# Kernel optimization log

Measured on AMD Instinct MI355X. Metric: run time of the kernel, lower is better.

## Reference

```python
import jax, jax.numpy as jnp
import numpy as np

N_NODES = 100000
N_EDGES = 1600000
IN_CH = 128
HID = 128
N_GRAPHS = 256


def gcn_conv(x, W, b, src, dst, n_nodes):
    """PyG GCNConv: linear -> symmetric degree normalization with self-loops -> scatter-add -> bias."""
    h = x @ W  # [N, H]
    # degree (in-degree on target index) including the added self-loop
    deg = 1.0 + jax.ops.segment_sum(jnp.ones((dst.shape[0],), x.dtype), dst, num_segments=n_nodes)
    dis = deg ** -0.5  # deg >= 1, no inf guard needed
    coef = dis[src] * dis[dst]  # [E]
    agg = jax.ops.segment_sum(h[src] * coef[:, None], dst, num_segments=n_nodes)
    # self-loop contribution: h[i] * dis[i]^2 = h[i] / deg[i]
    agg = agg + h * (1.0 / deg)[:, None]
    return agg + b


def global_mean_pool(x, batch, n_graphs):
    sums = jax.ops.segment_sum(x, batch, num_segments=n_graphs)
    cnts = jax.ops.segment_sum(jnp.ones((x.shape[0],), x.dtype), batch, num_segments=n_graphs)
    return sums / jnp.maximum(cnts, 1.0)[:, None]


def setup_inputs() -> dict:
    key = jax.random.key(0)
    ks = jax.random.split(key, 8)
    x = jax.random.normal(ks[0], (N_NODES, IN_CH), dtype=jnp.float32)
    edge_index = jax.random.randint(ks[1], (2, N_EDGES), 0, N_NODES, dtype=jnp.int32)
    batch = jnp.sort(jax.random.randint(ks[2], (N_NODES,), 0, N_GRAPHS, dtype=jnp.int32))
    # glorot-ish init for weights
    s1 = (6.0 / (IN_CH + HID)) ** 0.5
    W1 = jax.random.uniform(ks[3], (IN_CH, HID), jnp.float32, -s1, s1)
    b1 = jnp.zeros((HID,), jnp.float32)
    s2 = (6.0 / (HID + HID)) ** 0.5
    W2 = jax.random.uniform(ks[4], (HID, HID), jnp.float32, -s2, s2)
    b2 = jnp.zeros((HID,), jnp.float32)
    s3 = (6.0 / (HID + 1)) ** 0.5
    Wfc = jax.random.uniform(ks[5], (HID, 1), jnp.float32, -s3, s3)
    bfc = jnp.zeros((1,), jnp.float32)
    return {"x": x, "edge_index": edge_index, "batch": batch,
            "W1": W1, "b1": b1, "W2": W2, "b2": b2, "Wfc": Wfc, "bfc": bfc}


def reference(x, edge_index, batch, W1, b1, W2, b2, Wfc, bfc):
    src, dst = edge_index[0], edge_index[1]
    h = jax.nn.relu(gcn_conv(x, W1, b1, src, dst, N_NODES))
    h = jax.nn.relu(gcn_conv(h, W2, b2, src, dst, N_NODES))
    g = global_mean_pool(h, batch, N_GRAPHS)  # [G, H]
    out = g @ Wfc + bfc  # [G, 1]
    return out.squeeze(-1)
```

## Files before the change

kernel.cpp:

```cpp
#include <hip/hip_runtime.h>
#include <hip/hip_bf16.h>

#define N_NODES 100000
#define N_EDGES 1600000
#define HID 128
#define N_GRAPHS 256

#define BSHIFT 9
#define BSIZE 512
#define NBUCK ((N_NODES + BSIZE - 1) / BSIZE)
#define BCAP 14336
#define EPB 8192
#define NBLK_A ((N_EDGES + EPB - 1) / EPB)
#define ZOFF ((uint)N_NODES << 8)

typedef unsigned int uint;
typedef unsigned short ushort;
typedef short short8 __attribute__((ext_vector_type(8)));
typedef float f32x4 __attribute__((ext_vector_type(4)));

__device__ __forceinline__ ushort f2bf_hw(float f) {
    union { __hip_bfloat16 b; ushort u; } cv;
    cv.b = __float2bfloat16(f);
    return cv.u;
}
__device__ __forceinline__ uint4 pack8(const float* r) {
    uint4 o;
    o.x = (uint)f2bf_hw(r[0]) | ((uint)f2bf_hw(r[1]) << 16);
    o.y = (uint)f2bf_hw(r[2]) | ((uint)f2bf_hw(r[3]) << 16);
    o.z = (uint)f2bf_hw(r[4]) | ((uint)f2bf_hw(r[5]) << 16);
    o.w = (uint)f2bf_hw(r[6]) | ((uint)f2bf_hw(r[7]) << 16);
    return o;
}
__device__ __forceinline__ void accp(uint4 v, float2* a) {
    a[0].x += __uint_as_float(v.x << 16);
    a[0].y += __uint_as_float(v.x & 0xFFFF0000u);
    a[1].x += __uint_as_float(v.y << 16);
    a[1].y += __uint_as_float(v.y & 0xFFFF0000u);
    a[2].x += __uint_as_float(v.z << 16);
    a[2].y += __uint_as_float(v.z & 0xFFFF0000u);
    a[3].x += __uint_as_float(v.w << 16);
    a[3].y += __uint_as_float(v.w & 0xFFFF0000u);
}

union Frag16 {
    uint4 u;
    short8 s;
    ushort h[8];
};

__global__ void init_kernel(int* __restrict__ bfill, uint4* __restrict__ Azr,
                            uint4* __restrict__ Bzr) {
    int t = threadIdx.x;
    if (t < NBUCK) bfill[t] = 0;
    if (t < 16) Azr[t] = (uint4){0, 0, 0, 0};
    else if (t < 32) Bzr[t - 16] = (uint4){0, 0, 0, 0};
}

__global__ __launch_bounds__(256) void bucket_scatter_kernel(const int* __restrict__ src,
                                                             const int* __restrict__ dst,
                                                             int* __restrict__ bfill,
                                                             uint* __restrict__ bucketed) {
    __shared__ int h[NBUCK];
    __shared__ int rb[NBUCK];
    for (int t = threadIdx.x; t < NBUCK; t += 256) h[t] = 0;
    __syncthreads();
    int base = blockIdx.x * EPB;
#pragma unroll 4
    for (int it = 0; it < EPB / 256; ++it) {
        int e = base + it * 256 + threadIdx.x;
        if (e < N_EDGES) atomicAdd(&h[dst[e] >> BSHIFT], 1);
    }
    __syncthreads();
    for (int t = threadIdx.x; t < NBUCK; t += 256) {
        rb[t] = (h[t] ? atomicAdd(&bfill[t], h[t]) : 0) + t * BCAP;
        h[t] = 0;
    }
    __syncthreads();
#pragma unroll 4
    for (int it = 0; it < EPB / 256; ++it) {
        int e = base + it * 256 + threadIdx.x;
        if (e < N_EDGES) {
            int d = dst[e];
            int b = d >> BSHIFT;
            int pos = rb[b] + atomicAdd(&h[b], 1);
            bucketed[pos] = (uint)src[e] | ((uint)(d & (BSIZE - 1)) << 17);
        }
    }
}

__global__ __launch_bounds__(256) void bucket_csr_kernel(const uint* __restrict__ bucketed,
                                                         const int* __restrict__ bfill,
                                                         int* __restrict__ degi,
                                                         int* __restrict__ rowptr,
                                                         float* __restrict__ dis,
                                                         uint* __restrict__ csrb) {
    int b = blockIdx.x;
    int beg = b * BCAP;
    int ne = bfill[b];
    __shared__ int cnt[BSIZE];
    __shared__ int fl[BSIZE];
    __shared__ int ex[BSIZE];
    __shared__ int ps[256];
    int t = threadIdx.x;
    cnt[t] = 0; cnt[t + 256] = 0;
    fl[t] = 0;  fl[t + 256] = 0;
    __syncthreads();
    for (int i = t; i < ne; i += 256) atomicAdd(&cnt[bucketed[beg + i] >> 17], 1);
    __syncthreads();
    int v0 = cnt[2 * t], v1 = cnt[2 * t + 1];
    int p0 = (v0 + 15) & ~15;
    int p1 = (v1 + 15) & ~15;
    int s = p0 + p1;
    ps[t] = s;
    __syncthreads();
    for (int off = 1; off < 256; off <<= 1) {
        int a = (t >= off) ? ps[t - off] : 0;
        __syncthreads();
        ps[t] += a;
        __syncthreads();
    }
    int e0 = ps[t] - s;
    ex[2 * t] = e0;
    ex[2 * t + 1] = e0 + p0;
    int g = b * BSIZE + 2 * t;
    if (g < N_NODES) {
        degi[g] = p0; rowptr[g] = beg + e0;
        dis[g] = rsqrtf(1.0f + (float)v0);
    }
    if (g + 1 < N_NODES) {
        degi[g + 1] = p1; rowptr[g + 1] = beg + e0 + p0;
        dis[g + 1] = rsqrtf(1.0f + (float)v1);
    }
    __syncthreads();
    for (int i = t; i < ne; i += 256) {
        uint u = bucketed[beg + i];
        int dl = u >> 17;
        int p = ex[dl] + atomicAdd(&fl[dl], 1);
        csrb[beg + p] = (u & 0x1FFFFu) << 8;
    }
    __syncthreads();
    for (int p = v0; p < p0; ++p) csrb[beg + ex[2 * t] + p] = ZOFF;
    for (int p = v1; p < p1; ++p) csrb[beg + ex[2 * t + 1] + p] = ZOFF;
}

__global__ void prep_wfrag2(const float* __restrict__ W1, const float* __restrict__ W2,
                            uint4* __restrict__ WB1, uint4* __restrict__ WB2) {
    int t = blockIdx.x * 256 + threadIdx.x;
    if (t >= 4096) return;
    const float* W = (t < 2048) ? W1 : W2;
    uint4* WB = (t < 2048) ? WB1 : WB2;
    int tt = t & 2047;
    int lane = tt & 63;
    int nt = (tt >> 6) & 7;
    int kt = tt >> 9;
    int kbase = kt * 32 + (lane >> 4) * 8;
    int col = nt * 16 + (lane & 15);
    float r[8];
#pragma unroll
    for (int j = 0; j < 8; j++) r[j] = W[(size_t)(kbase + j) * 128 + col];
    WB[tt] = pack8(r);
}

template <bool F32IN>
__global__ __launch_bounds__(256) void mgemm_kernel(const void* __restrict__ Xv,
                                                    const uint4* __restrict__ WB,
                                                    const float* __restrict__ dis,
                                                    ushort* __restrict__ Y, int M) {
    __shared__ uint4 WBs[2048];
    __shared__ ushort stage[4][16][136];
#pragma unroll
    for (int i = 0; i < 8; i++) WBs[i * 256 + threadIdx.x] = WB[i * 256 + threadIdx.x];
    __syncthreads();

    int wave = threadIdx.x >> 6;
    int lane = threadIdx.x & 63;
    int r0 = blockIdx.x * 128 + wave * 32;
    if (r0 >= M) return;

    int rowA = lane & 15;
    int ksub = (lane >> 4) * 8;

    Frag16 a[2][4];
#pragma unroll
    for (int rt = 0; rt < 2; ++rt) {
        int row = r0 + rt * 16 + rowA;
        if (F32IN) {
            const float* xr = (const float*)Xv + (size_t)row * 128;
#pragma unroll
            for (int kt = 0; kt < 4; ++kt) {
                float4 lo = *(const float4*)(xr + kt * 32 + ksub);
                float4 hi = *(const float4*)(xr + kt * 32 + ksub + 4);
                float r[8] = {lo.x, lo.y, lo.z, lo.w, hi.x, hi.y, hi.z, hi.w};
                a[rt][kt].u = pack8(r);
            }
        } else {
            const uint4* xr = (const uint4*)Xv + (size_t)row * 16;
#pragma unroll
            for (int kt = 0; kt < 4; ++kt) a[rt][kt].u = xr[kt * 4 + (lane >> 4)];
        }
    }

    f32x4 acc[2][8];
#pragma unroll
    for (int rt = 0; rt < 2; ++rt)
#pragma unroll
        for (int nt = 0; nt < 8; ++nt) acc[rt][nt] = (f32x4){0.f, 0.f, 0.f, 0.f};

#pragma unroll
    for (int kt = 0; kt < 4; ++kt) {
#pragma unroll
        for (int nt = 0; nt < 8; ++nt) {
            Frag16 b;
            b.u = WBs[(kt * 8 + nt) * 64 + lane];
            acc[0][nt] = __builtin_amdgcn_mfma_f32_16x16x32_bf16(a[0][kt].s, b.s, acc[0][nt], 0, 0, 0);
            acc[1][nt] = __builtin_amdgcn_mfma_f32_16x16x32_bf16(a[1][kt].s, b.s, acc[1][nt], 0, 0, 0);
        }
    }

    int cbase = lane & 15;
    int rbl = (lane >> 4) * 4;
    ushort* sp = &stage[wave][0][0];
    char* Yb = (char*)Y;
#pragma unroll
    for (int rt = 0; rt < 2; ++rt) {
        int r0g = r0 + rt * 16;
        int rbase = r0g + rbl;
        float d0 = dis[rbase + 0], d1 = dis[rbase + 1];
        float d2 = dis[rbase + 2], d3 = dis[rbase + 3];
#pragma unroll
        for (int nt = 0; nt < 8; ++nt) {
            int col = nt * 16 + cbase;
            sp[(rbl + 0) * 136 + col] = f2bf_hw(acc[rt][nt][0] * d0);
            sp[(rbl + 1) * 136 + col] = f2bf_hw(acc[rt][nt][1] * d1);
            sp[(rbl + 2) * 136 + col] = f2bf_hw(acc[rt][nt][2] * d2);
            sp[(rbl + 3) * 136 + col] = f2bf_hw(acc[rt][nt][3] * d3);
        }
#pragma unroll
        for (int i = 0; i < 4; ++i) {
            int idx = i * 64 + lane;
            int row = idx >> 4, c16 = idx & 15;
            uint4 v = *(const uint4*)(sp + row * 136 + c16 * 8);
            *(uint4*)(Yb + (size_t)(r0g + row) * 256 + c16 * 16) = v;
        }
    }
}

template <int POOL>
__global__ __launch_bounds__(256) void aggregate_kernel(
    const ushort* __restrict__ T, const uint* __restrict__ csrb,
    const int* __restrict__ rowptr, const int* __restrict__ degi,
    const float* __restrict__ dis, const float* __restrict__ bias,
    ushort* __restrict__ H, const float* __restrict__ Wfc,
    float* __restrict__ ndot) {
    int wave = threadIdx.x >> 6;
    int node = blockIdx.x * 4 + wave;
    int lane = threadIdx.x & 63;
    int group = lane >> 4;
    uint sub16 = (uint)(lane & 15) * 16u;

    int start = rowptr[node];
    int iters = degi[node] >> 4;
    const char* Tb = (const char*)T;

    float2 acc[4];
#pragma unroll
    for (int i = 0; i < 4; i++) acc[i] = make_float2(0.f, 0.f);

    int jb = start + group;
    for (int it = 0; it < iters; ++it, jb += 16) {
        uint o0 = csrb[jb];
        uint o1 = csrb[jb + 4];
        uint o2 = csrb[jb + 8];
        uint o3 = csrb[jb + 12];
        uint4 v0 = *(const uint4*)(Tb + (o0 + sub16));
        uint4 v1 = *(const uint4*)(Tb + (o1 + sub16));
        uint4 v2 = *(const uint4*)(Tb + (o2 + sub16));
        uint4 v3 = *(const uint4*)(Tb + (o3 + sub16));
        accp(v0, acc); accp(v1, acc); accp(v2, acc); accp(v3, acc);
    }

#pragma unroll
    for (int i = 0; i < 4; i++) {
        acc[i].x += __shfl_xor(acc[i].x, 16);
        acc[i].y += __shfl_xor(acc[i].y, 16);
        acc[i].x += __shfl_xor(acc[i].x, 32);
        acc[i].y += __shfl_xor(acc[i].y, 32);
    }

    if (group == 0) {
        uint4 sv = *(const uint4*)(Tb + (((uint)node << 8) + sub16));
        accp(sv, acc);
        float di = dis[node];
        int sub = lane & 15;
        float4 blo = ((const float4*)bias)[sub * 2];
        float4 bhi = ((const float4*)bias)[sub * 2 + 1];
        float bb[8] = {blo.x, blo.y, blo.z, blo.w, bhi.x, bhi.y, bhi.z, bhi.w};
        float r[8];
        float af[8] = {acc[0].x, acc[0].y, acc[1].x, acc[1].y,
                       acc[2].x, acc[2].y, acc[3].x, acc[3].y};
#pragma unroll
        for (int i = 0; i < 8; i++) r[i] = fmaxf(di * af[i] + bb[i], 0.f);
        if (POOL == 0) {
            ((uint4*)H)[(size_t)node * 16 + sub] = pack8(r);
        } else {
            float4 wlo = ((const float4*)Wfc)[sub * 2];
            float4 whi = ((const float4*)Wfc)[sub * 2 + 1];
            float d = r[0] * wlo.x + r[1] * wlo.y + r[2] * wlo.z + r[3] * wlo.w
                    + r[4] * whi.x + r[5] * whi.y + r[6] * whi.z + r[7] * whi.w;
            d += __shfl_xor(d, 1);
            d += __shfl_xor(d, 2);
            d += __shfl_xor(d, 4);
            d += __shfl_xor(d, 8);
            if (sub == 0) ndot[node] = d;
        }
    }
}

__global__ __launch_bounds__(64) void pool_fc_kernel(const float* __restrict__ ndot,
                                                     const int* __restrict__ batch,
                                                     const float* __restrict__ bfc,
                                                     float* __restrict__ out) {
    int g = blockIdx.x;
    int lane = threadIdx.x;
    auto lb = [&](int key) {
        int lo = 0, hi = N_NODES;
        while (lo < hi) {
            int mid = (lo + hi) >> 1;
            if (batch[mid] < key) lo = mid + 1; else hi = mid;
        }
        return lo;
    };
    int a = lb(g), b = lb(g + 1);
    float s = 0.f;
    for (int i = a + lane; i < b; i += 64) s += ndot[i];
#pragma unroll
    for (int off = 32; off > 0; off >>= 1) s += __shfl_down(s, off);
    if (lane == 0) out[g] = s / fmaxf((float)(b - a), 1.0f) + bfc[0];
}

extern "C" void kernel_launch(void* const* d_in, const int* in_sizes, int n_in,
                              void* d_out, int out_size, void* d_ws, size_t ws_size,
                              hipStream_t stream) {
    const float* x    = (const float*)d_in[0];
    const int*   eidx = (const int*)d_in[1];
    const int*   batch= (const int*)d_in[2];
    const float* W1   = (const float*)d_in[3];
    const float* b1   = (const float*)d_in[4];
    const float* W2   = (const float*)d_in[5];
    const float* b2   = (const float*)d_in[6];
    const float* Wfc  = (const float*)d_in[7];
    const float* bfc  = (const float*)d_in[8];
    float* out = (float*)d_out;

    const int* src = eidx;
    const int* dst = eidx + N_EDGES;

    size_t off = 0;
    char* base = (char*)d_ws;
    auto alloc = [&](size_t bytes) -> void* {
        void* p = base + off;
        off += (bytes + 255) & ~(size_t)255;
        return p;
    };
    int*    bfill  = (int*)alloc(NBUCK * 4);
    ushort* A      = (ushort*)alloc((size_t)(N_NODES + 1) * HID * 2);
    ushort* B      = (ushort*)alloc((size_t)(N_NODES + 1) * HID * 2);
    int*    degi   = (int*)alloc(N_NODES * 4);
    int*    rowptr = (int*)alloc(N_NODES * 4);
    float*  dis    = (float*)alloc(N_NODES * 4);
    float*  ndot   = (float*)alloc(N_NODES * 4);
    uint*   csrb   = (uint*)alloc((size_t)NBUCK * BCAP * 4);
    uint*   bucketed = (uint*)alloc((size_t)NBUCK * BCAP * 4);
    uint4*  WB1    = (uint4*)alloc(2048 * 16);
    uint4*  WB2    = (uint4*)alloc(2048 * 16);

    init_kernel<<<1, 256, 0, stream>>>(bfill,
                                       (uint4*)(A + (size_t)N_NODES * HID),
                                       (uint4*)(B + (size_t)N_NODES * HID));

    bucket_scatter_kernel<<<NBLK_A, 256, 0, stream>>>(src, dst, bfill, bucketed);
    bucket_csr_kernel<<<NBUCK, 256, 0, stream>>>(bucketed, bfill, degi, rowptr, dis, csrb);

    prep_wfrag2<<<16, 256, 0, stream>>>(W1, W2, WB1, WB2);

    int gemm_grid = (N_NODES + 127) / 128;
    int agg_grid  = N_NODES / 4;

    mgemm_kernel<true><<<gemm_grid, 256, 0, stream>>>(x, WB1, dis, A, N_NODES);
    aggregate_kernel<0><<<agg_grid, 256, 0, stream>>>(A, csrb, rowptr, degi, dis, b1, B,
                                                      Wfc, ndot);
    mgemm_kernel<false><<<gemm_grid, 256, 0, stream>>>(B, WB2, dis, A, N_NODES);
    aggregate_kernel<1><<<agg_grid, 256, 0, stream>>>(A, csrb, rowptr, degi, dis, b2, B,
                                                      Wfc, ndot);

    pool_fc_kernel<<<N_GRAPHS, 64, 0, stream>>>(ndot, batch, bfc, out);
}
```

Baseline: 227.5 us.

## Fuse aggregation with GEMM via aggregate-then-transform and degree-sorted node permutation

Reorders each GCN layer to aggregate first and apply the weight matrix afterwards, so the MFMA GEMM runs inside the aggregation kernel on 16-node tiles staged in shared memory. The separate GEMM passes and their intermediate writes and reads disappear. Nodes are sorted into degree classes through a permutation so each block handles rows with similar edge counts, and CSR row padding drops from 16 to 4 to cut wasted gathers. Initialisation and weight-fragment prep are merged into one launch, at the cost of extra small histogram, scan and permutation kernels plus a shared-memory GEMM epilogue in each aggregation block.

```diff
diff --git a/kernel.cpp b/kernel.cpp
--- a/kernel.cpp
+++ b/kernel.cpp
@@ -9,9 +9,10 @@
 #define BSHIFT 9
 #define BSIZE 512
 #define NBUCK ((N_NODES + BSIZE - 1) / BSIZE)
-#define BCAP 14336
+#define BCAP 12288
 #define EPB 8192
 #define NBLK_A ((N_EDGES + EPB - 1) / EPB)
+#define NCLS 16
 #define ZOFF ((uint)N_NODES << 8)
 
 typedef unsigned int uint;
@@ -49,105 +50,20 @@
     ushort h[8];
 };
 
-__global__ void init_kernel(int* __restrict__ bfill, uint4* __restrict__ Azr,
-                            uint4* __restrict__ Bzr) {
-    int t = threadIdx.x;
-    if (t < NBUCK) bfill[t] = 0;
-    if (t < 16) Azr[t] = (uint4){0, 0, 0, 0};
-    else if (t < 32) Bzr[t - 16] = (uint4){0, 0, 0, 0};
-}
-
-__global__ __launch_bounds__(256) void bucket_scatter_kernel(const int* __restrict__ src,
-                                                             const int* __restrict__ dst,
-                                                             int* __restrict__ bfill,
-                                                             uint* __restrict__ bucketed) {
-    __shared__ int h[NBUCK];
-    __shared__ int rb[NBUCK];
-    for (int t = threadIdx.x; t < NBUCK; t += 256) h[t] = 0;
-    __syncthreads();
-    int base = blockIdx.x * EPB;
-#pragma unroll 4
-    for (int it = 0; it < EPB / 256; ++it) {
-        int e = base + it * 256 + threadIdx.x;
-        if (e < N_EDGES) atomicAdd(&h[dst[e] >> BSHIFT], 1);
-    }
-    __syncthreads();
-    for (int t = threadIdx.x; t < NBUCK; t += 256) {
-        rb[t] = (h[t] ? atomicAdd(&bfill[t], h[t]) : 0) + t * BCAP;
-        h[t] = 0;
-    }
-    __syncthreads();
-#pragma unroll 4
-    for (int it = 0; it < EPB / 256; ++it) {
-        int e = base + it * 256 + threadIdx.x;
-        if (e < N_EDGES) {
-            int d = dst[e];
-            int b = d >> BSHIFT;
-            int pos = rb[b] + atomicAdd(&h[b], 1);
-            bucketed[pos] = (uint)src[e] | ((uint)(d & (BSIZE - 1)) << 17);
-        }
-    }
-}
-
-__global__ __launch_bounds__(256) void bucket_csr_kernel(const uint* __restrict__ bucketed,
-                                                         const int* __restrict__ bfill,
-                                                         int* __restrict__ degi,
-                                                         int* __restrict__ rowptr,
-                                                         float* __restrict__ dis,
-                                                         uint* __restrict__ csrb) {
-    int b = blockIdx.x;
-    int beg = b * BCAP;
-    int ne = bfill[b];
-    __shared__ int cnt[BSIZE];
-    __shared__ int fl[BSIZE];
-    __shared__ int ex[BSIZE];
-    __shared__ int ps[256];
-    int t = threadIdx.x;
-    cnt[t] = 0; cnt[t + 256] = 0;
-    fl[t] = 0;  fl[t + 256] = 0;
-    __syncthreads();
-    for (int i = t; i < ne; i += 256) atomicAdd(&cnt[bucketed[beg + i] >> 17], 1);
-    __syncthreads();
-    int v0 = cnt[2 * t], v1 = cnt[2 * t + 1];
-    int p0 = (v0 + 15) & ~15;
-    int p1 = (v1 + 15) & ~15;
-    int s = p0 + p1;
-    ps[t] = s;
-    __syncthreads();
-    for (int off = 1; off < 256; off <<= 1) {
-        int a = (t >= off) ? ps[t - off] : 0;
-        __syncthreads();
-        ps[t] += a;
-        __syncthreads();
-    }
-    int e0 = ps[t] - s;
-    ex[2 * t] = e0;
-    ex[2 * t + 1] = e0 + p0;
-    int g = b * BSIZE + 2 * t;
-    if (g < N_NODES) {
-        degi[g] = p0; rowptr[g] = beg + e0;
-        dis[g] = rsqrtf(1.0f + (float)v0);
-    }
-    if (g + 1 < N_NODES) {
-        degi[g + 1] = p1; rowptr[g + 1] = beg + e0 + p0;
-        dis[g + 1] = rsqrtf(1.0f + (float)v1);
-    }
-    __syncthreads();
-    for (int i = t; i < ne; i += 256) {
-        uint u = bucketed[beg + i];
-        int dl = u >> 17;
-        int p = ex[dl] + atomicAdd(&fl[dl], 1);
-        csrb[beg + p] = (u & 0x1FFFFu) << 8;
-    }
-    __syncthreads();
-    for (int p = v0; p < p0; ++p) csrb[beg + ex[2 * t] + p] = ZOFF;
-    for (int p = v1; p < p1; ++p) csrb[beg + ex[2 * t + 1] + p] = ZOFF;
-}
-
-__global__ void prep_wfrag2(const float* __restrict__ W1, const float* __restrict__ W2,
-                            uint4* __restrict__ WB1, uint4* __restrict__ WB2) {
-    int t = blockIdx.x * 256 + threadIdx.x;
-    if (t >= 4096) return;
+__global__ void setup_kernel(int* __restrict__ bfill, int* __restrict__ clshist,
+                             int* __restrict__ clsfill,
+                             uint4* __restrict__ Azr, uint4* __restrict__ Bzr,
+                             const float* __restrict__ W1, const float* __restrict__ W2,
+                             uint4* __restrict__ WB1, uint4* __restrict__ WB2) {
+    if (blockIdx.x == 0) {
+        int t = threadIdx.x;
+        if (t < NBUCK) bfill[t] = 0;
+        if (t < NCLS) { clshist[t] = 0; clsfill[t] = 0; }
+        if (t < 16) Azr[t] = (uint4){0, 0, 0, 0};
+        else if (t < 32) Bzr[t - 16] = (uint4){0, 0, 0, 0};
+        return;
+    }
+    int t = (blockIdx.x - 1) * 256 + threadIdx.x;
     const float* W = (t < 2048) ? W1 : W2;
     uint4* WB = (t < 2048) ? WB1 : WB2;
     int tt = t & 2047;
@@ -162,157 +78,249 @@
     WB[tt] = pack8(r);
 }
 
-template <bool F32IN>
-__global__ __launch_bounds__(256) void mgemm_kernel(const void* __restrict__ Xv,
-                                                    const uint4* __restrict__ WB,
+__global__ __launch_bounds__(256) void bucket_scatter_kernel(const int* __restrict__ src,
+                                                             const int* __restrict__ dst,
+                                                             int* __restrict__ bfill,
+                                                             uint* __restrict__ bucketed) {
+    __shared__ int h[NBUCK];
+    __shared__ int rb[NBUCK];
+    for (int t = threadIdx.x; t < NBUCK; t += 256) h[t] = 0;
+    __syncthreads();
+    int base = blockIdx.x * EPB;
+#pragma unroll 4
+    for (int it = 0; it < EPB / 256; ++it) {
+        int e = base + it * 256 + threadIdx.x;
+        if (e < N_EDGES) atomicAdd(&h[dst[e] >> BSHIFT], 1);
+    }
+    __syncthreads();
+    for (int t = threadIdx.x; t < NBUCK; t += 256) {
+        rb[t] = (h[t] ? atomicAdd(&bfill[t], h[t]) : 0) + t * BCAP;
+        h[t] = 0;
+    }
+    __syncthreads();
+#pragma unroll 4
+    for (int it = 0; it < EPB / 256; ++it) {
+        int e = base + it * 256 + threadIdx.x;
+        if (e < N_EDGES) {
+            int d = dst[e];
+            int b = d >> BSHIFT;
+            int pos = rb[b] + atomicAdd(&h[b], 1);
+            bucketed[pos] = (uint)src[e] | ((uint)(d & (BSIZE - 1)) << 17);
+        }
+    }
+}
+
+__global__ __launch_bounds__(256) void bucket_csr_kernel(const uint* __restrict__ bucketed,
+                                                         const int* __restrict__ bfill,
+                                                         int* __restrict__ degi,
+                                                         int* __restrict__ rowptr,
+                                                         float* __restrict__ dis,
+                                                         uint* __restrict__ csrb,
+                                                         int* __restrict__ clshist) {
+    int b = blockIdx.x;
+    int beg = b * BCAP;
+    int ne = bfill[b];
+    __shared__ int cnt[BSIZE];
+    __shared__ int fl[BSIZE];
+    __shared__ int ex[BSIZE];
+    __shared__ int ps[256];
+    __shared__ int ch[NCLS];
+    int t = threadIdx.x;
+    cnt[t] = 0; cnt[t + 256] = 0;
+    fl[t] = 0;  fl[t + 256] = 0;
+    if (t < NCLS) ch[t] = 0;
+    __syncthreads();
+    for (int i = t; i < ne; i += 256) atomicAdd(&cnt[bucketed[beg + i] >> 17], 1);
+    __syncthreads();
+    int v0 = cnt[2 * t], v1 = cnt[2 * t + 1];
+    int p0 = (v0 + 3) & ~3;
+    int p1 = (v1 + 3) & ~3;
+    int s = p0 + p1;
+    ps[t] = s;
+    __syncthreads();
+    for (int off = 1; off < 256; off <<= 1) {
+        int a = (t >= off) ? ps[t - off] : 0;
+        __syncthreads();
+        ps[t] += a;
+        __syncthreads();
+    }
+    int e0 = ps[t] - s;
+    ex[2 * t] = e0;
+    ex[2 * t + 1] = e0 + p0;
+    int g = b * BSIZE + 2 * t;
+    if (g < N_NODES) {
+        degi[g] = p0; rowptr[g] = beg + e0;
+        dis[g] = rsqrtf(1.0f + (float)v0);
+        atomicAdd(&ch[min(p0 >> 2, NCLS - 1)], 1);
+    }
+    if (g + 1 < N_NODES) {
+        degi[g + 1] = p1; rowptr[g + 1] = beg + e0 + p0;
+        dis[g + 1] = rsqrtf(1.0f + (float)v1);
+        atomicAdd(&ch[min(p1 >> 2, NCLS - 1)], 1);
+    }
+    __syncthreads();
+    if (t < NCLS && ch[t]) atomicAdd(&clshist[t], ch[t]);
+    for (int i = t; i < ne; i += 256) {
+        uint u = bucketed[beg + i];
+        int dl = u >> 17;
+        int p = ex[dl] + atomicAdd(&fl[dl], 1);
+        csrb[beg + p] = (u & 0x1FFFFu) << 8;
+    }
+    __syncthreads();
+    for (int p = v0; p < p0; ++p) csrb[beg + ex[2 * t] + p] = ZOFF;
+    for (int p = v1; p < p1; ++p) csrb[beg + ex[2 * t + 1] + p] = ZOFF;
+}
+
+__global__ void clsbase_kernel(const int* __restrict__ clshist, int* __restrict__ clsbase) {
+    if (threadIdx.x == 0) {
+        int run = 0;
+        for (int c = 0; c < NCLS; ++c) { clsbase[c] = run; run += clshist[c]; }
+    }
+}
+
+__global__ __launch_bounds__(256) void perm_kernel(const int* __restrict__ degi,
+                                                   const int* __restrict__ clsbase,
+                                                   int* __restrict__ clsfill,
+                                                   int* __restrict__ perm) {
+    __shared__ int h[NCLS];
+    __shared__ int rb[NCLS];
+    int t = threadIdx.x;
+    if (t < NCLS) h[t] = 0;
+    __syncthreads();
+    int n = blockIdx.x * 256 + t;
+    int cls = 0, myloc = 0;
+    if (n < N_NODES) {
+        cls = min(degi[n] >> 2, NCLS - 1);
+        myloc = atomicAdd(&h[cls], 1);
+    }
+    __syncthreads();
+    if (t < NCLS) rb[t] = h[t] ? (clsbase[t] + atomicAdd(&clsfill[t], h[t])) : 0;
+    __syncthreads();
+    if (n < N_NODES) perm[rb[cls] + myloc] = n;
+}
+
+__global__ __launch_bounds__(256) void xprep_kernel(const float* __restrict__ x,
                                                     const float* __restrict__ dis,
-                                                    ushort* __restrict__ Y, int M) {
-    __shared__ uint4 WBs[2048];
-    __shared__ ushort stage[4][16][136];
-#pragma unroll
-    for (int i = 0; i < 8; i++) WBs[i * 256 + threadIdx.x] = WB[i * 256 + threadIdx.x];
-    __syncthreads();
-
-    int wave = threadIdx.x >> 6;
-    int lane = threadIdx.x & 63;
-    int r0 = blockIdx.x * 128 + wave * 32;
-    if (r0 >= M) return;
-
-    int rowA = lane & 15;
-    int ksub = (lane >> 4) * 8;
-
-    Frag16 a[2][4];
-#pragma unroll
-    for (int rt = 0; rt < 2; ++rt) {
-        int row = r0 + rt * 16 + rowA;
-        if (F32IN) {
-            const float* xr = (const float*)Xv + (size_t)row * 128;
-#pragma unroll
-            for (int kt = 0; kt < 4; ++kt) {
-                float4 lo = *(const float4*)(xr + kt * 32 + ksub);
-                float4 hi = *(const float4*)(xr + kt * 32 + ksub + 4);
-                float r[8] = {lo.x, lo.y, lo.z, lo.w, hi.x, hi.y, hi.z, hi.w};
-                a[rt][kt].u = pack8(r);
-            }
-        } else {
-            const uint4* xr = (const uint4*)Xv + (size_t)row * 16;
-#pragma unroll
-            for (int kt = 0; kt < 4; ++kt) a[rt][kt].u = xr[kt * 4 + (lane >> 4)];
-        }
-    }
-
-    f32x4 acc[2][8];
-#pragma unroll
-    for (int rt = 0; rt < 2; ++rt)
-#pragma unroll
-        for (int nt = 0; nt < 8; ++nt) acc[rt][nt] = (f32x4){0.f, 0.f, 0.f, 0.f};
-
-#pragma unroll
-    for (int kt = 0; kt < 4; ++kt) {
-#pragma unroll
-        for (int nt = 0; nt < 8; ++nt) {
-            Frag16 b;
-            b.u = WBs[(kt * 8 + nt) * 64 + lane];
-            acc[0][nt] = __builtin_amdgcn_mfma_f32_16x16x32_bf16(a[0][kt].s, b.s, acc[0][nt], 0, 0, 0);
-            acc[1][nt] = __builtin_amdgcn_mfma_f32_16x16x32_bf16(a[1][kt].s, b.s, acc[1][nt], 0, 0, 0);
-        }
-    }
-
-    int cbase = lane & 15;
-    int rbl = (lane >> 4) * 4;
-    ushort* sp = &stage[wave][0][0];
-    char* Yb = (char*)Y;
-#pragma unroll
-    for (int rt = 0; rt < 2; ++rt) {
-        int r0g = r0 + rt * 16;
-        int rbase = r0g + rbl;
-        float d0 = dis[rbase + 0], d1 = dis[rbase + 1];
-        float d2 = dis[rbase + 2], d3 = dis[rbase + 3];
-#pragma unroll
-        for (int nt = 0; nt < 8; ++nt) {
-            int col = nt * 16 + cbase;
-            sp[(rbl + 0) * 136 + col] = f2bf_hw(acc[rt][nt][0] * d0);
-            sp[(rbl + 1) * 136 + col] = f2bf_hw(acc[rt][nt][1] * d1);
-            sp[(rbl + 2) * 136 + col] = f2bf_hw(acc[rt][nt][2] * d2);
-            sp[(rbl + 3) * 136 + col] = f2bf_hw(acc[rt][nt][3] * d3);
-        }
-#pragma unroll
-        for (int i = 0; i < 4; ++i) {
-            int idx = i * 64 + lane;
-            int row = idx >> 4, c16 = idx & 15;
-            uint4 v = *(const uint4*)(sp + row * 136 + c16 * 8);
-            *(uint4*)(Yb + (size_t)(r0g + row) * 256 + c16 * 16) = v;
-        }
-    }
+                                                    uint4* __restrict__ Xp) {
+    int t = blockIdx.x * 256 + threadIdx.x;
+    if (t >= N_NODES * 16) return;
+    int n = t >> 4, c16 = t & 15;
+    const float* xr = x + (size_t)n * 128 + c16 * 8;
+    float d = dis[n];
+    float4 lo = *(const float4*)xr;
+    float4 hi = *(const float4*)(xr + 4);
+    float r[8] = {d * lo.x, d * lo.y, d * lo.z, d * lo.w,
+                  d * hi.x, d * hi.y, d * hi.z, d * hi.w};
+    Xp[t] = pack8(r);
 }
 
 template <int POOL>
-__global__ __launch_bounds__(256) void aggregate_kernel(
+__global__ __launch_bounds__(256, 8) void fused_agg_kernel(
     const ushort* __restrict__ T, const uint* __restrict__ csrb,
     const int* __restrict__ rowptr, const int* __restrict__ degi,
     const float* __restrict__ dis, const float* __restrict__ bias,
+    const int* __restrict__ perm, const uint4* __restrict__ WB,
     ushort* __restrict__ H, const float* __restrict__ Wfc,
     float* __restrict__ ndot) {
+    __shared__ ushort At[16][136];
+    __shared__ float disrow[16];
+    __shared__ int nid[16];
+    __shared__ float pdot[16][4];
+
     int wave = threadIdx.x >> 6;
-    int node = blockIdx.x * 4 + wave;
     int lane = threadIdx.x & 63;
     int group = lane >> 4;
-    uint sub16 = (uint)(lane & 15) * 16u;
-
+    int sub = lane & 15;
+    uint sub16 = (uint)sub * 16u;
+    int r = wave * 4 + group;
+    int node = perm[blockIdx.x * 16 + r];
     int start = rowptr[node];
-    int iters = degi[node] >> 4;
+    int iters = degi[node] >> 2;
     const char* Tb = (const char*)T;
 
     float2 acc[4];
 #pragma unroll
     for (int i = 0; i < 4; i++) acc[i] = make_float2(0.f, 0.f);
 
-    int jb = start + group;
-    for (int it = 0; it < iters; ++it, jb += 16) {
+    int jb = start;
+    for (int it = 0; it < iters; ++it, jb += 4) {
         uint o0 = csrb[jb];
-        uint o1 = csrb[jb + 4];
-        uint o2 = csrb[jb + 8];
-        uint o3 = csrb[jb + 12];
+        uint o1 = csrb[jb + 1];
+        uint o2 = csrb[jb + 2];
+        uint o3 = csrb[jb + 3];
         uint4 v0 = *(const uint4*)(Tb + (o0 + sub16));
         uint4 v1 = *(const uint4*)(Tb + (o1 + sub16));
         uint4 v2 = *(const uint4*)(Tb + (o2 + sub16));
         uint4 v3 = *(const uint4*)(Tb + (o3 + sub16));
         accp(v0, acc); accp(v1, acc); accp(v2, acc); accp(v3, acc);
     }
-
-#pragma unroll
-    for (int i = 0; i < 4; i++) {
-        acc[i].x += __shfl_xor(acc[i].x, 16);
-        acc[i].y += __shfl_xor(acc[i].y, 16);
-        acc[i].x += __shfl_xor(acc[i].x, 32);
-        acc[i].y += __shfl_xor(acc[i].y, 32);
-    }
-
-    if (group == 0) {
+    {
         uint4 sv = *(const uint4*)(Tb + (((uint)node << 8) + sub16));
         accp(sv, acc);
         float di = dis[node];
-        int sub = lane & 15;
-        float4 blo = ((const float4*)bias)[sub * 2];
-        float4 bhi = ((const float4*)bias)[sub * 2 + 1];
-        float bb[8] = {blo.x, blo.y, blo.z, blo.w, bhi.x, bhi.y, bhi.z, bhi.w};
-        float r[8];
-        float af[8] = {acc[0].x, acc[0].y, acc[1].x, acc[1].y,
-                       acc[2].x, acc[2].y, acc[3].x, acc[3].y};
-#pragma unroll
-        for (int i = 0; i < 8; i++) r[i] = fmaxf(di * af[i] + bb[i], 0.f);
-        if (POOL == 0) {
-            ((uint4*)H)[(size_t)node * 16 + sub] = pack8(r);
-        } else {
-            float4 wlo = ((const float4*)Wfc)[sub * 2];
-            float4 whi = ((const float4*)Wfc)[sub * 2 + 1];
-            float d = r[0] * wlo.x + r[1] * wlo.y + r[2] * wlo.z + r[3] * wlo.w
-                    + r[4] * whi.x + r[5] * whi.y + r[6] * whi.z + r[7] * whi.w;
-            d += __shfl_xor(d, 1);
-            d += __shfl_xor(d, 2);
-            d += __shfl_xor(d, 4);
-            d += __shfl_xor(d, 8);
-            if (sub == 0) ndot[node] = d;
+        float rr[8] = {di * acc[0].x, di * acc[0].y, di * acc[1].x, di * acc[1].y,
+                       di * acc[2].x, di * acc[2].y, di * acc[3].x, di * acc[3].y};
+        *(uint4*)&At[r][sub * 8] = pack8(rr);
+        if (sub == 0) { disrow[r] = di; nid[r] = node; }
+    }
+    __syncthreads();
+
+    Frag16 a[4];
+    int arow = lane & 15;
+    int achunk = lane >> 4;
+#pragma unroll
+    for (int kt = 0; kt < 4; ++kt)
+        a[kt].u = *(const uint4*)&At[arow][kt * 32 + achunk * 8];
+
+    f32x4 c0 = (f32x4){0.f, 0.f, 0.f, 0.f};
+    f32x4 c1 = (f32x4){0.f, 0.f, 0.f, 0.f};
+    int nt0 = wave * 2, nt1 = wave * 2 + 1;
+#pragma unroll
+    for (int kt = 0; kt < 4; ++kt) {
+        Frag16 b0, b1;
+        b0.u = WB[(kt * 8 + nt0) * 64 + lane];
+        b1.u = WB[(kt * 8 + nt1) * 64 + lane];
+        c0 = __builtin_amdgcn_mfma_f32_16x16x32_bf16(a[kt].s, b0.s, c0, 0, 0, 0);
+        c1 = __builtin_amdgcn_mfma_f32_16x16x32_bf16(a[kt].s, b1.s, c1, 0, 0, 0);
+    }
+
+    int col0 = nt0 * 16 + sub, col1 = nt1 * 16 + sub;
+    float b0s = bias[col0], b1s = bias[col1];
+    int rq = (lane >> 4) * 4;
+
+    if (POOL == 0) {
+        __syncthreads();
+#pragma unroll
+        for (int reg = 0; reg < 4; ++reg) {
+            float sc = disrow[rq + reg];
+            At[rq + reg][col0] = f2bf_hw(fmaxf(c0[reg] + b0s, 0.f) * sc);
+            At[rq + reg][col1] = f2bf_hw(fmaxf(c1[reg] + b1s, 0.f) * sc);
+        }
+        __syncthreads();
+        int row = threadIdx.x >> 4, c16 = threadIdx.x & 15;
+        uint4 v = *(const uint4*)&At[row][c16 * 8];
+        *(uint4*)((char*)H + (((size_t)(uint)nid[row]) << 8) + c16 * 16) = v;
+    } else {
+        float wf0 = Wfc[col0], wf1 = Wfc[col1];
+        float p[4];
+#pragma unroll
+        for (int reg = 0; reg < 4; ++reg)
+            p[reg] = fmaxf(c0[reg] + b0s, 0.f) * wf0 + fmaxf(c1[reg] + b1s, 0.f) * wf1;
+#pragma unroll
+        for (int reg = 0; reg < 4; ++reg) {
+            p[reg] += __shfl_xor(p[reg], 1);
+            p[reg] += __shfl_xor(p[reg], 2);
+            p[reg] += __shfl_xor(p[reg], 4);
+            p[reg] += __shfl_xor(p[reg], 8);
+        }
+        if (sub == 0) {
+#pragma unroll
+            for (int reg = 0; reg < 4; ++reg) pdot[rq + reg][wave] = p[reg];
+        }
+        __syncthreads();
+        if (threadIdx.x < 16) {
+            int row = threadIdx.x;
+            ndot[nid[row]] = pdot[row][0] + pdot[row][1] + pdot[row][2] + pdot[row][3];
         }
     }
 }
@@ -363,36 +371,41 @@
         off += (bytes + 255) & ~(size_t)255;
         return p;
     };
-    int*    bfill  = (int*)alloc(NBUCK * 4);
-    ushort* A      = (ushort*)alloc((size_t)(N_NODES + 1) * HID * 2);
-    ushort* B      = (ushort*)alloc((size_t)(N_NODES + 1) * HID * 2);
-    int*    degi   = (int*)alloc(N_NODES * 4);
-    int*    rowptr = (int*)alloc(N_NODES * 4);
-    float*  dis    = (float*)alloc(N_NODES * 4);
-    float*  ndot   = (float*)alloc(N_NODES * 4);
-    uint*   csrb   = (uint*)alloc((size_t)NBUCK * BCAP * 4);
-    uint*   bucketed = (uint*)alloc((size_t)NBUCK * BCAP * 4);
-    uint4*  WB1    = (uint4*)alloc(2048 * 16);
-    uint4*  WB2    = (uint4*)alloc(2048 * 16);
-
-    init_kernel<<<1, 256, 0, stream>>>(bfill,
-                                       (uint4*)(A + (size_t)N_NODES * HID),
-                                       (uint4*)(B + (size_t)N_NODES * HID));
+    int*    bfill   = (int*)alloc(NBUCK * 4);
+    int*    clshist = (int*)alloc(NCLS * 4);
+    int*    clsfill = (int*)alloc(NCLS * 4);
+    int*    clsbase = (int*)alloc(NCLS * 4);
+    ushort* A       = (ushort*)alloc((size_t)(N_NODES + 1) * HID * 2);
+    ushort* B       = (ushort*)alloc((size_t)(N_NODES + 1) * HID * 2);
+    int*    degi    = (int*)alloc(N_NODES * 4);
+    int*    rowptr  = (int*)alloc(N_NODES * 4);
+    float*  dis     = (float*)alloc(N_NODES * 4);
+    float*  ndot    = (float*)alloc(N_NODES * 4);
+    int*    perm    = (int*)alloc(N_NODES * 4);
+    uint*   csrb    = (uint*)alloc((size_t)NBUCK * BCAP * 4);
+    uint*   bucketed= (uint*)alloc((size_t)NBUCK * BCAP * 4);
+    uint4*  WB1     = (uint4*)alloc(2048 * 16);
+    uint4*  WB2     = (uint4*)alloc(2048 * 16);
+
+    setup_kernel<<<17, 256, 0, stream>>>(bfill, clshist, clsfill,
+                                         (uint4*)(A + (size_t)N_NODES * HID),
+                                         (uint4*)(B + (size_t)N_NODES * HID),
+                                         W1, W2, WB1, WB2);
 
     bucket_scatter_kernel<<<NBLK_A, 256, 0, stream>>>(src, dst, bfill, bucketed);
-    bucket_csr_kernel<<<NBUCK, 256, 0, stream>>>(bucketed, bfill, degi, rowptr, dis, csrb);
-
-    prep_wfrag2<<<16, 256, 0, stream>>>(W1, W2, WB1, WB2);
-
-    int gemm_grid = (N_NODES + 127) / 128;
-    int agg_grid  = N_NODES / 4;
-
-    mgemm_kernel<true><<<gemm_grid, 256, 0, stream>>>(x, WB1, dis, A, N_NODES);
-    aggregate_kernel<0><<<agg_grid, 256, 0, stream>>>(A, csrb, rowptr, degi, dis, b1, B,
-                                                      Wfc, ndot);
-    mgemm_kernel<false><<<gemm_grid, 256, 0, stream>>>(B, WB2, dis, A, N_NODES);
-    aggregate_kernel<1><<<agg_grid, 256, 0, stream>>>(A, csrb, rowptr, degi, dis, b2, B,
-                                                      Wfc, ndot);
+    bucket_csr_kernel<<<NBUCK, 256, 0, stream>>>(bucketed, bfill, degi, rowptr, dis,
+                                                 csrb, clshist);
+    clsbase_kernel<<<1, 64, 0, stream>>>(clshist, clsbase);
+    perm_kernel<<<(N_NODES + 255) / 256, 256, 0, stream>>>(degi, clsbase, clsfill, perm);
+
+    xprep_kernel<<<(N_NODES * 16 + 255) / 256, 256, 0, stream>>>(x, dis, (uint4*)A);
+
+    int fgrid = N_NODES / 16;
+
+    fused_agg_kernel<0><<<fgrid, 256, 0, stream>>>(A, csrb, rowptr, degi, dis, b1,
+                                                   perm, WB1, B, Wfc, ndot);
+    fused_agg_kernel<1><<<fgrid, 256, 0, stream>>>(B, csrb, rowptr, degi, dis, b2,
+                                                   perm, WB2, B, Wfc, ndot);
 
     pool_fc_kernel<<<N_GRAPHS, 64, 0, stream>>>(ndot, batch, bfc, out);
 }
```

Result: faster. 213.2 us (-6.3%).
